# Kernel tuning notes

Measured on AMD Instinct MI355X. Metric: run time of the kernel, lower is better.

## Reference

```python
import jax, jax.numpy as jnp
import numpy as np

NUM_POINTS = 32
NUM_RESIDUALS = 2
DIST_THRESHOLD = 5.0
H = W = 128
C = 16


def setup_inputs() -> dict:
    key = jax.random.key(0)
    k = jax.random.split(key, 6)
    return {
        "md_maps": jax.random.uniform(k[0], (1, 3, H, W), dtype=jnp.float32),
        "dis_maps": jax.random.uniform(k[1], (1, 1, H, W), dtype=jnp.float32),
        "residual_maps": jax.random.uniform(k[2], (1, 1, H, W), dtype=jnp.float32),
        "features": jax.random.normal(k[3], (C, H, W), dtype=jnp.float32),
        "jloc": jax.random.uniform(k[4], (1, H, W), dtype=jnp.float32),
        "joff": jax.random.uniform(k[5], (2, H, W), dtype=jnp.float32),
        "topk": 300,
    }


def hafm_decoding(md_maps, dis_maps, residual_maps):
    scale = DIST_THRESHOLD
    b, _, h, w = md_maps.shape
    y0, x0 = jnp.meshgrid(jnp.arange(h, dtype=jnp.float32),
                          jnp.arange(w, dtype=jnp.float32), indexing='ij')
    y0 = y0[None, None]
    x0 = x0[None, None]
    sign_pad = jnp.arange(-NUM_RESIDUALS, NUM_RESIDUALS + 1, dtype=jnp.float32).reshape(1, -1, 1, 1)
    dist = jnp.clip(dis_maps + residual_maps * sign_pad, 0.0, 1.0)  # [B, 2R+1, H, W]
    md_un = (md_maps[:, :1] - 0.5) * np.pi * 2.0
    st_un = md_maps[:, 1:2] * np.pi / 2.0
    ed_un = -md_maps[:, 2:3] * np.pi / 2.0
    cs_md = jnp.cos(md_un)
    ss_md = jnp.sin(md_un)
    y_st = jnp.tan(st_un)
    y_ed = jnp.tan(ed_un)
    x_st_final = jnp.clip((cs_md - ss_md * y_st) * dist * scale + x0, 0.0, w - 1)
    y_st_final = jnp.clip((ss_md + cs_md * y_st) * dist * scale + y0, 0.0, h - 1)
    x_ed_final = jnp.clip((cs_md - ss_md * y_ed) * dist * scale + x0, 0.0, w - 1)
    y_ed_final = jnp.clip((ss_md + cs_md * y_ed) * dist * scale + y0, 0.0, h - 1)
    lines = jnp.stack((x_st_final, y_st_final, x_ed_final, y_ed_final), axis=-1)
    return lines.reshape(b, -1, 4)  # [B, (2R+1)*H*W, 4]


def compute_loi_features(features_per_image, lines_per_im, tspan):
    c, h, w = features_per_image.shape
    U, V = lines_per_im[:, :2], lines_per_im[:, 2:]
    pts = U[:, :, None] * tspan + V[:, :, None] * (1.0 - tspan) - 0.5  # [N, 2, P]
    pts = pts.transpose(0, 2, 1).reshape(-1, 2)  # [N*P, 2]
    px, py = pts[:, 0], pts[:, 1]
    px0 = jnp.clip(jnp.floor(px), 0.0, w - 1)
    py0 = jnp.clip(jnp.floor(py), 0.0, h - 1)
    px1 = jnp.clip(px0 + 1.0, 0.0, w - 1)
    py1 = jnp.clip(py0 + 1.0, 0.0, h - 1)
    px0l, py0l = px0.astype(jnp.int32), py0.astype(jnp.int32)
    px1l, py1l = px1.astype(jnp.int32), py1.astype(jnp.int32)
    xp = (features_per_image[:, py0l, px0l] * (py1 - py) * (px1 - px)
          + features_per_image[:, py1l, px0l] * (py - py0) * (px1 - px)
          + features_per_image[:, py0l, px1l] * (py1 - py) * (px - px0)
          + features_per_image[:, py1l, px1l] * (py - py0) * (px - px0))  # [C, N*P]
    xp = xp.reshape(c, -1, tspan.size).transpose(1, 0, 2)  # [N, C, P]
    return xp.reshape(xp.shape[0], -1)  # [N, C*P]


def non_maximum_suppression(a):
    # a: [B, 1, H, W]; torch max_pool2d pads with -inf for max pooling
    ap = jax.lax.reduce_window(a, -jnp.inf, jax.lax.max, (1, 1, 3, 3), (1, 1, 1, 1),
                               [(0, 0), (0, 0), (1, 1), (1, 1)])
    return a * (a == ap).astype(a.dtype)


def get_junctions(jloc, joff, topk):
    h, w = jloc.shape[-2], jloc.shape[-1]
    flat = jloc.reshape(-1)
    joff2 = joff.reshape(2, -1)
    scores, index = jax.lax.top_k(flat, topk)
    y = (index // w).astype(jnp.float32) + joff2[1][index] + 0.5
    x = (index % w).astype(jnp.float32) + joff2[0][index] + 0.5
    junctions = jnp.stack((x, y), axis=1)  # [topk, 2]
    return junctions, scores


def reference(md_maps, dis_maps, residual_maps, features, jloc, joff, topk):
    tspan = jnp.linspace(0.0, 1.0, NUM_POINTS, dtype=jnp.float32)[None, None, :]
    lines = hafm_decoding(md_maps, dis_maps, residual_maps)  # [1, 5*H*W, 4]
    loi = compute_loi_features(features, lines[0], tspan)    # [5*H*W, C*P]
    jloc_nms = non_maximum_suppression(jloc[None])            # [1, 1, H, W]
    junctions, scores = get_junctions(jloc_nms[0], joff, topk)
    return loi, junctions, scores
```

## Files before the change

kernel.cpp:

```cpp
#include <hip/hip_runtime.h>
#include <math.h>

#define HPX 128
#define WPX 128
#define HW  16384
#define CCH 16
#define NLINES 81920
#define NPTS 32
#define LOI_SIZE (NLINES * 512)
#define NBINS 4096
#define CAND 1024
#define PREP_TRANS (HW * CCH)
#define PREP_TOTAL (PREP_TRANS + NLINES + HW)

#define FEAT_T_OFF 0
#define LINES_OFF  1048576
#define KEYS_OFF   (1048576 + 1310720)

__global__ __launch_bounds__(256) void prep_kernel(
        const float* __restrict__ feat, float* __restrict__ feat_t,
        const float* __restrict__ md,
        const float* __restrict__ dis,
        const float* __restrict__ res,
        float4* __restrict__ lines,
        const float* __restrict__ jloc,
        unsigned long long* __restrict__ keys_full) {
    int tid = blockIdx.x * 256 + threadIdx.x;

    if (tid < PREP_TRANS) {
        int pix = tid >> 4;
        int c   = tid & 15;
        feat_t[tid] = feat[c * HW + pix];
    } else if (tid < PREP_TRANS + NLINES) {
        int line = tid - PREP_TRANS;
        int r    = line >> 14;
        int pix  = line & (HW - 1);
        int y0i  = pix >> 7, x0i = pix & 127;

        float md0 = md[pix], md1 = md[HW + pix], md2 = md[2 * HW + pix];
        float dv  = dis[pix], rv = res[pix];

        float dist = fminf(fmaxf(dv + rv * ((float)r - 2.0f), 0.0f), 1.0f);
        float d5   = dist * 5.0f;
        float md_un = (md0 - 0.5f) * 6.28318530717958647692f;
        float cs = cosf(md_un), ss = sinf(md_un);
        float y_st = tanf(md1 * 1.57079632679489661923f);
        float y_ed = tanf(-md2 * 1.57079632679489661923f);

        float x0f = (float)x0i, y0f = (float)y0i;
        float4 ep;
        ep.x = fminf(fmaxf((cs - ss * y_st) * d5 + x0f, 0.0f), 127.0f);
        ep.y = fminf(fmaxf((ss + cs * y_st) * d5 + y0f, 0.0f), 127.0f);
        ep.z = fminf(fmaxf((cs - ss * y_ed) * d5 + x0f, 0.0f), 127.0f);
        ep.w = fminf(fmaxf((ss + cs * y_ed) * d5 + y0f, 0.0f), 127.0f);
        lines[line] = ep;
    } else {
        int pix = tid - PREP_TRANS - NLINES;
        int y = pix >> 7, x = pix & 127;
        float a = jloc[pix];
        float m = a;
        #pragma unroll
        for (int dy = -1; dy <= 1; dy++) {
            #pragma unroll
            for (int dx = -1; dx <= 1; dx++) {
                int yy = y + dy, xx = x + dx;
                if (yy >= 0 && yy < HPX && xx >= 0 && xx < WPX) {
                    m = fmaxf(m, jloc[yy * WPX + xx]);
                }
            }
        }
        unsigned long long kk = 0ull;
        if (a == m && a > 0.0f) {
            kk = ((unsigned long long)__float_as_uint(a) << 32)
               | (unsigned long long)(0xFFFFFFFFu - (unsigned int)pix);
        }
        keys_full[pix] = kk;
    }
}

__global__ __launch_bounds__(1024) void select_topk(
        const unsigned long long* __restrict__ keys_full,
        const float* __restrict__ joff,
        float* __restrict__ junc, float* __restrict__ scores, int topk) {
    __shared__ unsigned int h[NBINS];
    __shared__ unsigned long long cand[CAND];
    __shared__ unsigned int wt[16];
    __shared__ unsigned int wo[16];
    __shared__ unsigned int scount;
    __shared__ int Ts;
    int t = threadIdx.x;
    int l = t & 63, w = t >> 6;

    #pragma unroll
    for (int r = 0; r < 4; r++) h[t * 4 + r] = 0u;
    if (t == 0) { scount = 0; Ts = 0; }
    __syncthreads();

    #pragma unroll
    for (int i = 0; i < 16; i++) {
        unsigned long long kk = keys_full[t + i * 1024];
        if (kk) {
            float val = __uint_as_float((unsigned int)(kk >> 32));
            int bin = min(NBINS - 1, (int)(val * (float)NBINS));
            atomicAdd(&h[bin], 1u);
        }
    }
    __syncthreads();

    unsigned int h0 = h[4 * t], h1 = h[4 * t + 1],
                 h2 = h[4 * t + 2], h3 = h[4 * t + 3];
    unsigned int s3 = h3, s2 = h2 + s3, s1 = h1 + s2, s0 = h0 + s1;

    unsigned int x = s0;
    #pragma unroll
    for (int off = 1; off < 64; off <<= 1) {
        unsigned int y = __shfl_down(x, off);
        if (l + off < 64) x += y;
    }
    if (l == 0) wt[w] = x;
    __syncthreads();
    if (t < 16) {
        unsigned int acc = 0;
        for (int ww = 15; ww > t; ww--) acc += wt[ww];
        wo[t] = acc;
    }
    __syncthreads();

    unsigned int A  = wo[w] + (x - s0);
    unsigned int S0 = s0 + A, S1 = s1 + A, S2 = s2 + A, S3 = s3 + A;
    unsigned int tku = (unsigned int)topk;
    if (S0 >= tku && S1 < tku) Ts = 4 * t;
    if (S1 >= tku && S2 < tku) Ts = 4 * t + 1;
    if (S2 >= tku && S3 < tku) Ts = 4 * t + 2;
    if (S3 >= tku && A  < tku) Ts = 4 * t + 3;
    __syncthreads();
    int T = Ts;

    #pragma unroll
    for (int i = 0; i < 16; i++) {
        unsigned long long kk = keys_full[t + i * 1024];
        if (kk) {
            float val = __uint_as_float((unsigned int)(kk >> 32));
            int bin = min(NBINS - 1, (int)(val * (float)NBINS));
            if (bin >= T) {
                unsigned int p = atomicAdd(&scount, 1u);
                if (p < CAND) cand[p] = kk;
            }
        }
    }
    __syncthreads();
    unsigned int sc = min(scount, (unsigned int)CAND);

    if (t < (int)sc) {
        unsigned long long k = cand[t];
        int r = 0;
        for (unsigned int j = 0; j < sc; j++) r += (cand[j] > k) ? 1 : 0;
        if (r < topk) {
            float val = __uint_as_float((unsigned int)(k >> 32));
            unsigned int idx = 0xFFFFFFFFu - (unsigned int)(k & 0xFFFFFFFFull);
            if (idx >= HW) idx = 0;
            float xo = joff[idx];
            float yo = joff[HW + idx];
            junc[2 * r]     = (float)(idx & 127) + xo + 0.5f;
            junc[2 * r + 1] = (float)(idx >> 7)  + yo + 0.5f;
            scores[r] = val;
        }
    }
    if (t >= (int)sc && t < topk) {
        junc[2 * t]     = joff[0] + 0.5f;
        junc[2 * t + 1] = joff[HW] + 0.5f;
        scores[t] = 0.0f;
    }
}

__global__ __launch_bounds__(256) void loi_kernel(
        const float4* __restrict__ lines,
        const float4* __restrict__ feat4,
        float* __restrict__ out) {
    int tid  = blockIdx.x * 256 + threadIdx.x;
    int cq   = tid & 3;
    int p    = (tid >> 2) & 31;
    int line = tid >> 7;

    float4 ep = lines[line];

    float tk = (float)p * (1.0f / 31.0f);
    float px = ep.x * tk + ep.z * (1.0f - tk) - 0.5f;
    float py = ep.y * tk + ep.w * (1.0f - tk) - 0.5f;

    float px0 = fminf(fmaxf(floorf(px), 0.0f), 127.0f);
    float py0 = fminf(fmaxf(floorf(py), 0.0f), 127.0f);
    float px1 = fminf(px0 + 1.0f, 127.0f);
    float py1 = fminf(py0 + 1.0f, 127.0f);

    float wx1 = px - px0, wx0 = px1 - px;
    float wy1 = py - py0, wy0 = py1 - py;
    float w00 = wy0 * wx0, w01 = wy0 * wx1;
    float w10 = wy1 * wx0, w11 = wy1 * wx1;

    int r0 = ((int)py0) * WPX;
    int r1 = ((int)py1) * WPX;
    int c0 = (int)px0;
    int c1 = (int)px1;

    float4 a = feat4[(r0 + c0) * 4 + cq];
    float4 b = feat4[(r0 + c1) * 4 + cq];
    float4 c = feat4[(r1 + c0) * 4 + cq];
    float4 d = feat4[(r1 + c1) * 4 + cq];

    float v0 = a.x * w00 + b.x * w01 + c.x * w10 + d.x * w11;
    float v1 = a.y * w00 + b.y * w01 + c.y * w10 + d.y * w11;
    float v2 = a.z * w00 + b.z * w01 + c.z * w10 + d.z * w11;
    float v3 = a.w * w00 + b.w * w01 + c.w * w10 + d.w * w11;

    float* ob = out + (size_t)line * 512 + cq * 128 + p;
    __builtin_nontemporal_store(v0, ob);
    __builtin_nontemporal_store(v1, ob + 32);
    __builtin_nontemporal_store(v2, ob + 64);
    __builtin_nontemporal_store(v3, ob + 96);
}

extern "C" void kernel_launch(void* const* d_in, const int* in_sizes, int n_in,
                              void* d_out, int out_size, void* d_ws, size_t ws_size,
                              hipStream_t stream) {
    const float* md   = (const float*)d_in[0];
    const float* dis  = (const float*)d_in[1];
    const float* res  = (const float*)d_in[2];
    const float* feat = (const float*)d_in[3];
    const float* jloc = (const float*)d_in[4];
    const float* joff = (const float*)d_in[5];
    int topk = (out_size - LOI_SIZE) / 3;

    char* ws = (char*)d_ws;
    float* feat_t                 = (float*)(ws + FEAT_T_OFF);
    float4* lines                 = (float4*)(ws + LINES_OFF);
    unsigned long long* keys_full = (unsigned long long*)(ws + KEYS_OFF);

    float* out    = (float*)d_out;
    float* junc   = out + LOI_SIZE;
    float* scores = junc + 2 * topk;

    prep_kernel <<<PREP_TOTAL / 256, 256, 0, stream>>>(
                    feat, feat_t, md, dis, res, lines, jloc, keys_full);
    select_topk <<<1, 1024, 0, stream>>>(keys_full, joff, junc, scores, topk);
    loi_kernel  <<<(NLINES * 128) / 256, 256, 0, stream>>>(
                    lines, (const float4*)feat_t, out);
}
```

Measured before the change: 216.5 us.

## Fuse line decoding and top-k into LOI kernel, compact NMS survivors in shared memory

Drops the lines buffer and the keys buffer. Each LOI thread now recomputes the line endpoints from the md, dis and res maps, which repeats the trig math for all 128 threads of a line. Block 0 of the fused launch performs NMS and top-k selection, compacting survivors into shared memory, so that work overlaps with the LOI blocks and one launch is saved. Blocks grow to 1024 threads, and the redundant sin, cos and tan per thread add ALU work to a store-bound kernel.

```diff
diff --git a/kernel.cpp b/kernel.cpp
--- a/kernel.cpp
+++ b/kernel.cpp
@@ -6,140 +6,108 @@
 #define HW  16384
 #define CCH 16
 #define NLINES 81920
-#define NPTS 32
 #define LOI_SIZE (NLINES * 512)
 #define NBINS 4096
 #define CAND 1024
-#define PREP_TRANS (HW * CCH)
-#define PREP_TOTAL (PREP_TRANS + NLINES + HW)
+#define SURV_CAP 4096
 
 #define FEAT_T_OFF 0
-#define LINES_OFF  1048576
-#define KEYS_OFF   (1048576 + 1310720)
-
-__global__ __launch_bounds__(256) void prep_kernel(
-        const float* __restrict__ feat, float* __restrict__ feat_t,
+
+__global__ __launch_bounds__(256) void transpose_feat(
+        const float* __restrict__ feat, float* __restrict__ feat_t) {
+    int tid = blockIdx.x * 256 + threadIdx.x;
+    int pix = tid >> 4;
+    int c   = tid & 15;
+    feat_t[tid] = feat[c * HW + pix];
+}
+
+__global__ __launch_bounds__(1024) void fused_kernel(
         const float* __restrict__ md,
         const float* __restrict__ dis,
         const float* __restrict__ res,
-        float4* __restrict__ lines,
+        const float4* __restrict__ feat4,
         const float* __restrict__ jloc,
-        unsigned long long* __restrict__ keys_full) {
-    int tid = blockIdx.x * 256 + threadIdx.x;
-
-    if (tid < PREP_TRANS) {
-        int pix = tid >> 4;
-        int c   = tid & 15;
-        feat_t[tid] = feat[c * HW + pix];
-    } else if (tid < PREP_TRANS + NLINES) {
-        int line = tid - PREP_TRANS;
-        int r    = line >> 14;
-        int pix  = line & (HW - 1);
-        int y0i  = pix >> 7, x0i = pix & 127;
-
-        float md0 = md[pix], md1 = md[HW + pix], md2 = md[2 * HW + pix];
-        float dv  = dis[pix], rv = res[pix];
-
-        float dist = fminf(fmaxf(dv + rv * ((float)r - 2.0f), 0.0f), 1.0f);
-        float d5   = dist * 5.0f;
-        float md_un = (md0 - 0.5f) * 6.28318530717958647692f;
-        float cs = cosf(md_un), ss = sinf(md_un);
-        float y_st = tanf(md1 * 1.57079632679489661923f);
-        float y_ed = tanf(-md2 * 1.57079632679489661923f);
-
-        float x0f = (float)x0i, y0f = (float)y0i;
-        float4 ep;
-        ep.x = fminf(fmaxf((cs - ss * y_st) * d5 + x0f, 0.0f), 127.0f);
-        ep.y = fminf(fmaxf((ss + cs * y_st) * d5 + y0f, 0.0f), 127.0f);
-        ep.z = fminf(fmaxf((cs - ss * y_ed) * d5 + x0f, 0.0f), 127.0f);
-        ep.w = fminf(fmaxf((ss + cs * y_ed) * d5 + y0f, 0.0f), 127.0f);
-        lines[line] = ep;
-    } else {
-        int pix = tid - PREP_TRANS - NLINES;
-        int y = pix >> 7, x = pix & 127;
-        float a = jloc[pix];
-        float m = a;
+        const float* __restrict__ joff,
+        float* __restrict__ out,
+        float* __restrict__ junc,
+        float* __restrict__ scores, int topk) {
+
+    if (blockIdx.x == 0) {
+        __shared__ unsigned int h[NBINS];
+        __shared__ unsigned long long surv[SURV_CAP];
+        __shared__ unsigned long long cand[CAND];
+        __shared__ unsigned int wt[16];
+        __shared__ unsigned int wo[16];
+        __shared__ unsigned int nsurv, scount;
+        __shared__ int Ts;
+        int t = threadIdx.x;
+        int l = t & 63, w = t >> 6;
+
         #pragma unroll
-        for (int dy = -1; dy <= 1; dy++) {
+        for (int r = 0; r < 4; r++) h[t * 4 + r] = 0u;
+        if (t == 0) { nsurv = 0; scount = 0; Ts = 0; }
+        __syncthreads();
+
+        #pragma unroll
+        for (int i = 0; i < 16; i++) {
+            int pix = t + i * 1024;
+            int y = pix >> 7, x = pix & 127;
+            float a = jloc[pix];
+            float m = a;
             #pragma unroll
-            for (int dx = -1; dx <= 1; dx++) {
-                int yy = y + dy, xx = x + dx;
-                if (yy >= 0 && yy < HPX && xx >= 0 && xx < WPX) {
-                    m = fmaxf(m, jloc[yy * WPX + xx]);
+            for (int dy = -1; dy <= 1; dy++) {
+                #pragma unroll
+                for (int dx = -1; dx <= 1; dx++) {
+                    int yy = y + dy, xx = x + dx;
+                    if (yy >= 0 && yy < HPX && xx >= 0 && xx < WPX) {
+                        m = fmaxf(m, jloc[yy * WPX + xx]);
+                    }
                 }
             }
-        }
-        unsigned long long kk = 0ull;
-        if (a == m && a > 0.0f) {
-            kk = ((unsigned long long)__float_as_uint(a) << 32)
-               | (unsigned long long)(0xFFFFFFFFu - (unsigned int)pix);
-        }
-        keys_full[pix] = kk;
-    }
-}
-
-__global__ __launch_bounds__(1024) void select_topk(
-        const unsigned long long* __restrict__ keys_full,
-        const float* __restrict__ joff,
-        float* __restrict__ junc, float* __restrict__ scores, int topk) {
-    __shared__ unsigned int h[NBINS];
-    __shared__ unsigned long long cand[CAND];
-    __shared__ unsigned int wt[16];
-    __shared__ unsigned int wo[16];
-    __shared__ unsigned int scount;
-    __shared__ int Ts;
-    int t = threadIdx.x;
-    int l = t & 63, w = t >> 6;
-
-    #pragma unroll
-    for (int r = 0; r < 4; r++) h[t * 4 + r] = 0u;
-    if (t == 0) { scount = 0; Ts = 0; }
-    __syncthreads();
-
-    #pragma unroll
-    for (int i = 0; i < 16; i++) {
-        unsigned long long kk = keys_full[t + i * 1024];
-        if (kk) {
-            float val = __uint_as_float((unsigned int)(kk >> 32));
-            int bin = min(NBINS - 1, (int)(val * (float)NBINS));
-            atomicAdd(&h[bin], 1u);
-        }
-    }
-    __syncthreads();
-
-    unsigned int h0 = h[4 * t], h1 = h[4 * t + 1],
-                 h2 = h[4 * t + 2], h3 = h[4 * t + 3];
-    unsigned int s3 = h3, s2 = h2 + s3, s1 = h1 + s2, s0 = h0 + s1;
-
-    unsigned int x = s0;
-    #pragma unroll
-    for (int off = 1; off < 64; off <<= 1) {
-        unsigned int y = __shfl_down(x, off);
-        if (l + off < 64) x += y;
-    }
-    if (l == 0) wt[w] = x;
-    __syncthreads();
-    if (t < 16) {
-        unsigned int acc = 0;
-        for (int ww = 15; ww > t; ww--) acc += wt[ww];
-        wo[t] = acc;
-    }
-    __syncthreads();
-
-    unsigned int A  = wo[w] + (x - s0);
-    unsigned int S0 = s0 + A, S1 = s1 + A, S2 = s2 + A, S3 = s3 + A;
-    unsigned int tku = (unsigned int)topk;
-    if (S0 >= tku && S1 < tku) Ts = 4 * t;
-    if (S1 >= tku && S2 < tku) Ts = 4 * t + 1;
-    if (S2 >= tku && S3 < tku) Ts = 4 * t + 2;
-    if (S3 >= tku && A  < tku) Ts = 4 * t + 3;
-    __syncthreads();
-    int T = Ts;
-
-    #pragma unroll
-    for (int i = 0; i < 16; i++) {
-        unsigned long long kk = keys_full[t + i * 1024];
-        if (kk) {
+            if (a == m && a > 0.0f) {
+                unsigned long long kk =
+                    ((unsigned long long)__float_as_uint(a) << 32)
+                  | (unsigned long long)(0xFFFFFFFFu - (unsigned int)pix);
+                unsigned int p = atomicAdd(&nsurv, 1u);
+                if (p < SURV_CAP) surv[p] = kk;
+                int bin = min(NBINS - 1, (int)(a * (float)NBINS));
+                atomicAdd(&h[bin], 1u);
+            }
+        }
+        __syncthreads();
+
+        unsigned int h0 = h[4 * t], h1 = h[4 * t + 1],
+                     h2 = h[4 * t + 2], h3 = h[4 * t + 3];
+        unsigned int s3 = h3, s2 = h2 + s3, s1 = h1 + s2, s0 = h0 + s1;
+
+        unsigned int x = s0;
+        #pragma unroll
+        for (int off = 1; off < 64; off <<= 1) {
+            unsigned int y = __shfl_down(x, off);
+            if (l + off < 64) x += y;
+        }
+        if (l == 0) wt[w] = x;
+        __syncthreads();
+        if (t < 16) {
+            unsigned int acc = 0;
+            for (int ww = 15; ww > t; ww--) acc += wt[ww];
+            wo[t] = acc;
+        }
+        __syncthreads();
+
+        unsigned int A  = wo[w] + (x - s0);
+        unsigned int S0 = s0 + A, S1 = s1 + A, S2 = s2 + A, S3 = s3 + A;
+        unsigned int tku = (unsigned int)topk;
+        if (S0 >= tku && S1 < tku) Ts = 4 * t;
+        if (S1 >= tku && S2 < tku) Ts = 4 * t + 1;
+        if (S2 >= tku && S3 < tku) Ts = 4 * t + 2;
+        if (S3 >= tku && A  < tku) Ts = 4 * t + 3;
+        __syncthreads();
+        int T = Ts;
+
+        unsigned int ns = min(nsurv, (unsigned int)SURV_CAP);
+        for (unsigned int i = t; i < ns; i += 1024) {
+            unsigned long long kk = surv[i];
             float val = __uint_as_float((unsigned int)(kk >> 32));
             int bin = min(NBINS - 1, (int)(val * (float)NBINS));
             if (bin >= T) {
@@ -147,42 +115,57 @@
                 if (p < CAND) cand[p] = kk;
             }
         }
+        __syncthreads();
+        unsigned int sc = min(scount, (unsigned int)CAND);
+
+        if (t < (int)sc) {
+            unsigned long long k = cand[t];
+            int r = 0;
+            for (unsigned int j = 0; j < sc; j++) r += (cand[j] > k) ? 1 : 0;
+            if (r < topk) {
+                float val = __uint_as_float((unsigned int)(k >> 32));
+                unsigned int idx = 0xFFFFFFFFu - (unsigned int)(k & 0xFFFFFFFFull);
+                if (idx >= HW) idx = 0;
+                float xo = joff[idx];
+                float yo = joff[HW + idx];
+                junc[2 * r]     = (float)(idx & 127) + xo + 0.5f;
+                junc[2 * r + 1] = (float)(idx >> 7)  + yo + 0.5f;
+                scores[r] = val;
+            }
+        }
+        if (t >= (int)sc && t < topk) {
+            junc[2 * t]     = joff[0] + 0.5f;
+            junc[2 * t + 1] = joff[HW] + 0.5f;
+            scores[t] = 0.0f;
+        }
+        return;
     }
-    __syncthreads();
-    unsigned int sc = min(scount, (unsigned int)CAND);
-
-    if (t < (int)sc) {
-        unsigned long long k = cand[t];
-        int r = 0;
-        for (unsigned int j = 0; j < sc; j++) r += (cand[j] > k) ? 1 : 0;
-        if (r < topk) {
-            float val = __uint_as_float((unsigned int)(k >> 32));
-            unsigned int idx = 0xFFFFFFFFu - (unsigned int)(k & 0xFFFFFFFFull);
-            if (idx >= HW) idx = 0;
-            float xo = joff[idx];
-            float yo = joff[HW + idx];
-            junc[2 * r]     = (float)(idx & 127) + xo + 0.5f;
-            junc[2 * r + 1] = (float)(idx >> 7)  + yo + 0.5f;
-            scores[r] = val;
-        }
-    }
-    if (t >= (int)sc && t < topk) {
-        junc[2 * t]     = joff[0] + 0.5f;
-        junc[2 * t + 1] = joff[HW] + 0.5f;
-        scores[t] = 0.0f;
-    }
-}
-
-__global__ __launch_bounds__(256) void loi_kernel(
-        const float4* __restrict__ lines,
-        const float4* __restrict__ feat4,
-        float* __restrict__ out) {
-    int tid  = blockIdx.x * 256 + threadIdx.x;
+
+    int tid  = (blockIdx.x - 1) * 1024 + threadIdx.x;
     int cq   = tid & 3;
     int p    = (tid >> 2) & 31;
     int line = tid >> 7;
 
-    float4 ep = lines[line];
+    int r    = line >> 14;
+    int pix  = line & (HW - 1);
+    int y0i  = pix >> 7, x0i = pix & 127;
+
+    float md0 = md[pix], md1 = md[HW + pix], md2 = md[2 * HW + pix];
+    float dv  = dis[pix], rv = res[pix];
+
+    float dist = fminf(fmaxf(dv + rv * ((float)r - 2.0f), 0.0f), 1.0f);
+    float d5   = dist * 5.0f;
+    float md_un = (md0 - 0.5f) * 6.28318530717958647692f;
+    float cs = cosf(md_un), ss = sinf(md_un);
+    float y_st = tanf(md1 * 1.57079632679489661923f);
+    float y_ed = tanf(-md2 * 1.57079632679489661923f);
+
+    float x0f = (float)x0i, y0f = (float)y0i;
+    float4 ep;
+    ep.x = fminf(fmaxf((cs - ss * y_st) * d5 + x0f, 0.0f), 127.0f);
+    ep.y = fminf(fmaxf((ss + cs * y_st) * d5 + y0f, 0.0f), 127.0f);
+    ep.z = fminf(fmaxf((cs - ss * y_ed) * d5 + x0f, 0.0f), 127.0f);
+    ep.w = fminf(fmaxf((ss + cs * y_ed) * d5 + y0f, 0.0f), 127.0f);
 
     float tk = (float)p * (1.0f / 31.0f);
     float px = ep.x * tk + ep.z * (1.0f - tk) - 0.5f;
@@ -232,17 +215,14 @@
     int topk = (out_size - LOI_SIZE) / 3;
 
     char* ws = (char*)d_ws;
-    float* feat_t                 = (float*)(ws + FEAT_T_OFF);
-    float4* lines                 = (float4*)(ws + LINES_OFF);
-    unsigned long long* keys_full = (unsigned long long*)(ws + KEYS_OFF);
+    float* feat_t = (float*)(ws + FEAT_T_OFF);
 
     float* out    = (float*)d_out;
     float* junc   = out + LOI_SIZE;
     float* scores = junc + 2 * topk;
 
-    prep_kernel <<<PREP_TOTAL / 256, 256, 0, stream>>>(
-                    feat, feat_t, md, dis, res, lines, jloc, keys_full);
-    select_topk <<<1, 1024, 0, stream>>>(keys_full, joff, junc, scores, topk);
-    loi_kernel  <<<(NLINES * 128) / 256, 256, 0, stream>>>(
-                    lines, (const float4*)feat_t, out);
+    transpose_feat<<<(HW * CCH) / 256, 256, 0, stream>>>(feat, feat_t);
+    fused_kernel  <<<1 + (NLINES * 128) / 1024, 1024, 0, stream>>>(
+                      md, dis, res, (const float4*)feat_t, jloc, joff,
+                      out, junc, scores, topk);
 }
```

Result: slower. 225.4 us (+4.1%).
